# Kernel optimization log

Hardware: AMD Instinct MI355X
Metric: run time of the kernel (lower is better)

## Reference

```python
import math
import jax, jax.numpy as jnp
import numpy as np

N, L, D = 64, 128, 768          # batch, n_in capsules, feature dim
IN_DIM, OUT_DIM, N_OUT = 64, 64, 32
EPS = 1e-8

def _xavier(k, shape):
    # torch xavier_uniform: fan_in = shape[1]*prod(shape[2:]), fan_out = shape[0]*prod(shape[2:])
    rec = int(np.prod(shape[2:])) if len(shape) > 2 else 1
    fan_in, fan_out = shape[-2] * rec, shape[-1] * rec
    a = math.sqrt(6.0 / (fan_in + fan_out))
    return jax.random.uniform(k, shape, jnp.float32, -a, a)

def setup_inputs() -> dict:
    key = jax.random.key(0)
    ks = jax.random.split(key, 4)
    return {
        "x": jax.random.normal(ks[0], (N, L, D), jnp.float32),
        "Wscore": _xavier(ks[1], (L, D, 1)),
        "Bscore": jnp.zeros((L, 1, 1), jnp.float32),
        "Wcap": _xavier(ks[2], (L, D, IN_DIM)),
        "Bcap": jnp.zeros((L, 1, IN_DIM), jnp.float32),
        "Wvote": _xavier(ks[3], (L, N_OUT, IN_DIM, OUT_DIM)),
        "Bvote": jnp.zeros((L, N_OUT, 1, OUT_DIM), jnp.float32),
        "beta_use": jnp.zeros((L, 1, 1, 1), jnp.float32),
        "beta_ign": jnp.zeros((1, N_OUT, 1, 1), jnp.float32),
        "iters": 3,
    }

def reference(x, Wscore, Bscore, Wcap, Bcap, Wvote, Bvote, beta_use, beta_ign, iters):
    n_out = Wvote.shape[1]
    pi = jnp.asarray(math.pi, x.dtype)
    x_t = jnp.transpose(x, (1, 0, 2))                     # (L, N, D)
    a_in = jnp.matmul(x_t, Wscore) + Bscore               # (L, N, 1)
    mu_in = jax.nn.gelu(jnp.matmul(x_t, Wcap) + Bcap, approximate=False)  # (L, N, in_dim)
    f_a_in = jax.nn.sigmoid(a_in)[:, None, :, :]          # (L, 1, N, 1)
    # votes: (L, n_out, N, out_dim)
    V = jnp.einsum('lni,loij->lonj', mu_in, Wvote) + Bvote

    def em_step(R):
        D_use = f_a_in * R                                # (L, n_out, N, 1)
        D_ign = f_a_in - D_use
        a_out = jnp.sum(beta_use * D_use, axis=0) - jnp.sum(beta_ign * D_ign, axis=0)  # (n_out, N, 1)
        denom = jnp.sum(D_use, axis=0) + EPS              # (n_out, N, 1)
        mu_out = jnp.sum(D_use * V, axis=0) / denom       # (n_out, N, out_dim)
        var_out = jnp.sum(D_use * (V - mu_out[None]) ** 2, axis=0) / denom
        return a_out, mu_out, var_out

    R = jnp.full((1, n_out, 1, 1), 1.0 / n_out, dtype=x.dtype)
    a_out, mu_out, var_out = em_step(R)
    for _ in range(int(iters) - 1):
        # Gaussian log-likelihood of each vote under each output capsule
        log_p = (-jnp.sum((V - mu_out[None]) ** 2 / (2.0 * var_out[None] + EPS), axis=-1)
                 - 1.0 - 0.5 * pi
                 - 0.5 * jnp.sum(jnp.log(var_out[None] + EPS), axis=-1))   # (L, n_out, N)
        R = jax.nn.softmax(jax.nn.log_sigmoid(a_out)[None] + log_p[..., None], axis=1)
        a_out, mu_out, var_out = em_step(R)

    a_out = jnp.transpose(a_out[..., 0], (1, 0))          # (N, n_out)
    mu_out = jnp.transpose(mu_out, (1, 0, 2))             # (N, n_out, out_dim)
    return a_out, mu_out
```

## Files before the change

kernel.cpp:

```cpp
#include <hip/hip_runtime.h>
#include <math.h>

#define NB 64
#define LL 128
#define DD 768
#define ID 64
#define OD 64
#define NO 32
#define EPSF 1e-8f

typedef unsigned short ushort_t;
typedef __attribute__((ext_vector_type(8))) short bf16x8;
typedef __attribute__((ext_vector_type(4))) float f32x4;


__device__ __forceinline__ float gelu_exact(float v) {
  return 0.5f * v * (1.0f + erff(v * 0.70710678118654752440f));
}
__device__ __forceinline__ float sigmoidf_(float z) {
  return 1.0f / (1.0f + __expf(-z));
}
__device__ __forceinline__ unsigned short f2bf(float f) {
  unsigned u = __float_as_uint(f);
  unsigned r = (u + 0x7FFFu + ((u >> 16) & 1u)) >> 16;
  return (unsigned short)r;
}
__device__ __forceinline__ float bf2f(unsigned short s) {
  return __uint_as_float(((unsigned)s) << 16);
}

__global__ __launch_bounds__(256) void k0a_proj(
    const float* __restrict__ x, const float* __restrict__ Wscore,
    const float* __restrict__ Wcap,
    float* __restrict__ Cpart, float* __restrict__ apart)
{
  const int l  = blockIdx.x & 127;
  const int kc = blockIdx.x >> 7;
  const int t = threadIdx.x;
  const int tn = t >> 4;
  const int ti = t & 15;
  __shared__ float Xs[64][68];
  __shared__ float Ws[64][68];
  __shared__ float Ss[64];
  float C[4][4] = {{0.f}};
  float asum[4] = {0.f, 0.f, 0.f, 0.f};

  for (int kt = 0; kt < 2; ++kt) {
    const int kbase = kc * 128 + kt * 64;
#pragma unroll
    for (int r = 0; r < 4; ++r) {
      const int flat = r * 1024 + t * 4;
      const int p = flat >> 6, qq = flat & 63;
      *(float4*)&Xs[p][qq] = *(const float4*)&x[(p * LL + l) * DD + kbase + qq];
      *(float4*)&Ws[p][qq] = *(const float4*)&Wcap[(l * DD + kbase + p) * ID + qq];
    }
    if (t < 16)
      *(float4*)&Ss[4 * t] = *(const float4*)&Wscore[l * DD + kbase + 4 * t];
    __syncthreads();
#pragma unroll 8
    for (int k = 0; k < 64; ++k) {
      float av[4];
      av[0] = Xs[4 * tn + 0][k];
      av[1] = Xs[4 * tn + 1][k];
      av[2] = Xs[4 * tn + 2][k];
      av[3] = Xs[4 * tn + 3][k];
      const float4 b = *(const float4*)&Ws[k][4 * ti];
      const float sk = Ss[k];
#pragma unroll
      for (int a = 0; a < 4; ++a) {
        C[a][0] = fmaf(av[a], b.x, C[a][0]);
        C[a][1] = fmaf(av[a], b.y, C[a][1]);
        C[a][2] = fmaf(av[a], b.z, C[a][2]);
        C[a][3] = fmaf(av[a], b.w, C[a][3]);
        asum[a] = fmaf(av[a], sk, asum[a]);
      }
    }
    __syncthreads();
  }
#pragma unroll
  for (int a = 0; a < 4; ++a)
    *(float4*)&Cpart[kc * 524288 + (l * 64 + 4 * tn + a) * 64 + 4 * ti] =
        make_float4(C[a][0], C[a][1], C[a][2], C[a][3]);
  if (ti == 0) {
#pragma unroll
    for (int a = 0; a < 4; ++a)
      apart[kc * 8192 + l * 64 + 4 * tn + a] = asum[a];
  }
}

__global__ __launch_bounds__(256) void k0b_reduce(
    const float* __restrict__ Cpart, const float* __restrict__ Bcap,
    ushort_t* __restrict__ Ah, ushort_t* __restrict__ Al)
{
  const int e = (blockIdx.x * 256 + threadIdx.x) * 4;
  float4 s = *(const float4*)&Cpart[e];
#pragma unroll
  for (int kc = 1; kc < 6; ++kc) {
    const float4 p = *(const float4*)&Cpart[kc * 524288 + e];
    s.x += p.x; s.y += p.y; s.z += p.z; s.w += p.w;
  }
  const int l = e >> 12;
  const int col = e & 63;
  const float4 bc = *(const float4*)&Bcap[l * 64 + col];
  float m[4] = {gelu_exact(s.x + bc.x), gelu_exact(s.y + bc.y),
                gelu_exact(s.z + bc.z), gelu_exact(s.w + bc.w)};
  ushort4 h, lo;
  h.x = f2bf(m[0]); lo.x = f2bf(m[0] - bf2f(h.x));
  h.y = f2bf(m[1]); lo.y = f2bf(m[1] - bf2f(h.y));
  h.z = f2bf(m[2]); lo.z = f2bf(m[2] - bf2f(h.z));
  h.w = f2bf(m[3]); lo.w = f2bf(m[3] - bf2f(h.w));
  *(ushort4*)&Ah[e] = h;
  *(ushort4*)&Al[e] = lo;
}

__global__ __launch_bounds__(256) void k0c_fa(
    const float* __restrict__ apart, const float* __restrict__ Bscore,
    float* __restrict__ f_a)
{
  const int e = blockIdx.x * 256 + threadIdx.x;
  float s = 0.f;
#pragma unroll
  for (int kc = 0; kc < 6; ++kc) s += apart[kc * 8192 + e];
  const int l = e >> 6;
  f_a[e] = sigmoidf_(s + Bscore[l]);
}

__global__ __launch_bounds__(256) void k1_votes(
    const ushort_t* __restrict__ Ah, const ushort_t* __restrict__ Al,
    const float* __restrict__ Wvote, const float* __restrict__ Bvote,
    float* __restrict__ V)
{
  const int t = threadIdx.x;
  const int w = t >> 6;
  const int lane = t & 63;
  const int pair = blockIdx.x * 4 + w;
  const int l = pair >> 5;
  const int mr = lane & 15, q = lane >> 4;

  __shared__ unsigned HL_all[4][2048];
  unsigned* HL = HL_all[w];

  bf16x8 afh[2][4], afl[2][4];
#pragma unroll
  for (int ks = 0; ks < 2; ++ks)
#pragma unroll
    for (int mt = 0; mt < 4; ++mt) {
      const int off = l * 4096 + (16 * mt + mr) * 64 + ks * 32 + q * 8;
      afh[ks][mt] = *(const bf16x8*)&Ah[off];
      afl[ks][mt] = *(const bf16x8*)&Al[off];
    }

  const float* Wt = Wvote + (size_t)pair * 4096;

  f32x4 acc[4][4];
#pragma unroll
  for (int mt = 0; mt < 4; ++mt)
#pragma unroll
    for (int nt = 0; nt < 4; ++nt) {
      f32x4 z = {0.f, 0.f, 0.f, 0.f};
      acc[mt][nt] = z;
    }

  for (int ks = 0; ks < 2; ++ks) {
#pragma unroll
    for (int f = 0; f < 8; ++f) {
      const float4 v4 = *(const float4*)&Wt[ks * 2048 + f * 256 + lane * 4];
      const int ii = f * 4 + q;
      const int jc = (mr * 4) ^ ((ii & 8) << 1);
      const float e4[4] = {v4.x, v4.y, v4.z, v4.w};
      unsigned pk[4];
#pragma unroll
      for (int d = 0; d < 4; ++d) {
        const unsigned short hi = f2bf(e4[d]);
        const unsigned short lo = f2bf(e4[d] - bf2f(hi));
        pk[d] = (unsigned)hi | ((unsigned)lo << 16);
      }
      *(uint4*)&HL[ii * 64 + jc] = make_uint4(pk[0], pk[1], pk[2], pk[3]);
    }

#pragma unroll
    for (int nt = 0; nt < 4; ++nt) {
      const int j = 16 * nt + mr;
      unsigned wv[8];
#pragma unroll
      for (int d = 0; d < 8; ++d) {
        const int ii = q * 8 + d;
        wv[d] = HL[ii * 64 + (j ^ ((ii & 8) << 1))];
      }
      union { ushort_t u[8]; bf16x8 v; } bh, bl;
#pragma unroll
      for (int d = 0; d < 8; ++d) {
        bh.u[d] = (ushort_t)(wv[d] & 0xffffu);
        bl.u[d] = (ushort_t)(wv[d] >> 16);
      }
#pragma unroll
      for (int mt = 0; mt < 4; ++mt) {
        acc[mt][nt] = __builtin_amdgcn_mfma_f32_16x16x32_bf16(
            afh[ks][mt], bh.v, acc[mt][nt], 0, 0, 0);
        acc[mt][nt] = __builtin_amdgcn_mfma_f32_16x16x32_bf16(
            afh[ks][mt], bl.v, acc[mt][nt], 0, 0, 0);
        acc[mt][nt] = __builtin_amdgcn_mfma_f32_16x16x32_bf16(
            afl[ks][mt], bh.v, acc[mt][nt], 0, 0, 0);
      }
    }
  }

  float bv[4];
#pragma unroll
  for (int nt = 0; nt < 4; ++nt) bv[nt] = Bvote[pair * 64 + 16 * nt + mr];

#pragma unroll
  for (int mt = 0; mt < 4; ++mt)
#pragma unroll
    for (int r = 0; r < 4; ++r) {
      const int n = 16 * mt + 4 * q + r;
      const size_t base = (size_t)n * (LL * NO * OD) + (size_t)pair * 64;
#pragma unroll
      for (int nt = 0; nt < 4; ++nt)
        V[base + 16 * nt + mr] = acc[mt][nt][r] + bv[nt];
    }
}

__global__ __launch_bounds__(256) void k3_em(
    const float* __restrict__ V, const float* __restrict__ f_a,
    const float* __restrict__ beta_use, const float* __restrict__ mu_s,
    const float* __restrict__ i2v_s, const float* __restrict__ cterm,
    float* __restrict__ S1p, float* __restrict__ S2p,
    float* __restrict__ dnp, float* __restrict__ aUp, const int mode)
{
  const int n = blockIdx.x >> 3;
  const int c = blockIdx.x & 7;
  const int t = threadIdx.x;
  const int o = t >> 3, q = t & 7;
  __shared__ float ttl[8][32];

  float mu8[8], iv8[8];
  float ct = 0.f;
  if (mode) {
    const float4 a0 = *(const float4*)&mu_s[n * 2048 + t * 8];
    const float4 a1 = *(const float4*)&mu_s[n * 2048 + t * 8 + 4];
    mu8[0] = a0.x; mu8[1] = a0.y; mu8[2] = a0.z; mu8[3] = a0.w;
    mu8[4] = a1.x; mu8[5] = a1.y; mu8[6] = a1.z; mu8[7] = a1.w;
    const float4 b0 = *(const float4*)&i2v_s[n * 2048 + t * 8];
    const float4 b1 = *(const float4*)&i2v_s[n * 2048 + t * 8 + 4];
    iv8[0] = b0.x; iv8[1] = b0.y; iv8[2] = b0.z; iv8[3] = b0.w;
    iv8[4] = b1.x; iv8[5] = b1.y; iv8[6] = b1.z; iv8[7] = b1.w;
    ct = cterm[n * NO + o];
  }
  float aS1[8] = {0.f, 0.f, 0.f, 0.f, 0.f, 0.f, 0.f, 0.f};
  float aS2[8] = {0.f, 0.f, 0.f, 0.f, 0.f, 0.f, 0.f, 0.f};
  float dn = 0.f, aU = 0.f;

  for (int g = 0; g < 4; ++g) {
    const int lb = c * 16 + g * 4;
    float Vv[4][8], fa4[4], bu4[4], tt4[4];
#pragma unroll
    for (int u = 0; u < 4; ++u) {
      const int l = lb + u;
      const float4 v0 = *(const float4*)&V[((size_t)n * LL + l) * 2048 + t * 8];
      const float4 v1 = *(const float4*)&V[((size_t)n * LL + l) * 2048 + t * 8 + 4];
      Vv[u][0] = v0.x; Vv[u][1] = v0.y; Vv[u][2] = v0.z; Vv[u][3] = v0.w;
      Vv[u][4] = v1.x; Vv[u][5] = v1.y; Vv[u][6] = v1.z; Vv[u][7] = v1.w;
      fa4[u] = f_a[l * NB + n];
      bu4[u] = beta_use[l];
    }
    if (mode) {
#pragma unroll
      for (int u = 0; u < 4; ++u) {
        float s2 = 0.f;
#pragma unroll
        for (int k = 0; k < 8; ++k) {
          const float d = Vv[u][k] - mu8[k];
          s2 = fmaf(d * d, iv8[k], s2);
        }
        s2 += __shfl_xor(s2, 1);
        s2 += __shfl_xor(s2, 2);
        s2 += __shfl_xor(s2, 4);
        tt4[u] = ct - s2;
      }
      const int sb = (g & 1) * 4;
      if (q == 0) {
#pragma unroll
        for (int u = 0; u < 4; ++u) ttl[sb + u][o] = tt4[u];
      }
      __syncthreads();
#pragma unroll
      for (int u = 0; u < 4; ++u) {
        const float vv = ttl[sb + u][t & 31];
        float m = vv;
#pragma unroll
        for (int msk = 1; msk <= 16; msk <<= 1) m = fmaxf(m, __shfl_xor(m, msk));
        float z = __expf(vv - m);
#pragma unroll
        for (int msk = 1; msk <= 16; msk <<= 1) z += __shfl_xor(z, msk);
        const float wgt = fa4[u] * __expf(tt4[u] - m) / z;
        dn += wgt;
        aU = fmaf(bu4[u], wgt, aU);
#pragma unroll
        for (int k = 0; k < 8; ++k) {
          const float d = Vv[u][k] - mu8[k];
          aS1[k] = fmaf(wgt, Vv[u][k], aS1[k]);
          aS2[k] = fmaf(wgt, d * d, aS2[k]);
        }
      }
    } else {
#pragma unroll
      for (int u = 0; u < 4; ++u) {
        const float wgt = fa4[u] * (1.0f / NO);
        dn += wgt;
        aU = fmaf(bu4[u], wgt, aU);
#pragma unroll
        for (int k = 0; k < 8; ++k) {
          aS1[k] = fmaf(wgt, Vv[u][k], aS1[k]);
          aS2[k] = fmaf(wgt * Vv[u][k], Vv[u][k], aS2[k]);
        }
      }
    }
  }
  const int base = ((c * NB + n) * NO + o) * OD + q * 8;
  *(float4*)&S1p[base]     = make_float4(aS1[0], aS1[1], aS1[2], aS1[3]);
  *(float4*)&S1p[base + 4] = make_float4(aS1[4], aS1[5], aS1[6], aS1[7]);
  *(float4*)&S2p[base]     = make_float4(aS2[0], aS2[1], aS2[2], aS2[3]);
  *(float4*)&S2p[base + 4] = make_float4(aS2[4], aS2[5], aS2[6], aS2[7]);
  if (q == 0) {
    dnp[(c * NB + n) * NO + o] = dn;
    aUp[(c * NB + n) * NO + o] = aU;
  }
}

__global__ __launch_bounds__(256) void k4_fin23(
    const float* __restrict__ S1p, const float* __restrict__ S2p,
    const float* __restrict__ dnp, const float* __restrict__ aUp,
    const float* __restrict__ f_a, const float* __restrict__ beta_ign,
    float* __restrict__ mu_s, float* __restrict__ i2v_s, float* __restrict__ cterm,
    float* __restrict__ out, const int final_iter, const int first)
{
  const int n = blockIdx.x;
  const int t = threadIdx.x;
  const int o = t >> 3, q = t & 7;
  const int j0 = q * 8;
  __shared__ float rA[128];
  if (t < 128) rA[t] = f_a[t * NB + n];
  __syncthreads();
  for (int s = 64; s >= 1; s >>= 1) {
    if (t < s) rA[t] += rA[t + s];
    __syncthreads();
  }
  const float Fsum = rA[0];

  float dn = 0.f, aU = 0.f;
#pragma unroll
  for (int cc = 0; cc < 8; ++cc) {
    dn += dnp[(cc * NB + n) * NO + o];
    aU += aUp[(cc * NB + n) * NO + o];
  }
  const float S0 = dn;
  const float denom = dn + EPSF;
  const float inv_den = 1.0f / denom;

  float S1[8], S2[8];
#pragma unroll
  for (int k = 0; k < 8; ++k) { S1[k] = 0.f; S2[k] = 0.f; }
  for (int cc = 0; cc < 8; ++cc) {
    const int base = ((cc * NB + n) * NO + o) * OD + j0;
    const float4 u0 = *(const float4*)&S1p[base];
    const float4 u1 = *(const float4*)&S1p[base + 4];
    const float4 w0 = *(const float4*)&S2p[base];
    const float4 w1 = *(const float4*)&S2p[base + 4];
    S1[0] += u0.x; S1[1] += u0.y; S1[2] += u0.z; S1[3] += u0.w;
    S1[4] += u1.x; S1[5] += u1.y; S1[6] += u1.z; S1[7] += u1.w;
    S2[0] += w0.x; S2[1] += w0.y; S2[2] += w0.z; S2[3] += w0.w;
    S2[4] += w1.x; S2[5] += w1.y; S2[6] += w1.z; S2[7] += w1.w;
  }
  float mup[8];
  if (first) {
#pragma unroll
    for (int k = 0; k < 8; ++k) mup[k] = 0.f;
  } else {
    const float4 a0 = *(const float4*)&mu_s[n * 2048 + t * 8];
    const float4 a1 = *(const float4*)&mu_s[n * 2048 + t * 8 + 4];
    mup[0] = a0.x; mup[1] = a0.y; mup[2] = a0.z; mup[3] = a0.w;
    mup[4] = a1.x; mup[5] = a1.y; mup[6] = a1.z; mup[7] = a1.w;
  }
  const float aout = aU - beta_ign[o] * (Fsum - dn);

  float mu[8], i2v[8];
  float lacc = 0.f;
#pragma unroll
  for (int k = 0; k < 8; ++k) {
    mu[k] = S1[k] * inv_den;
    const float dd = mu[k] - mup[k];
    float varn = S2[k] - 2.0f * dd * (S1[k] - mup[k] * S0) + dd * dd * S0;
    float var = fmaxf(varn * inv_den, 0.0f);
    i2v[k] = 1.0f / (2.0f * var + EPSF);
    lacc += logf(var + EPSF);
  }
  if (final_iter) {
    if (q == 0) out[n * NO + o] = aout;
    *(float4*)&out[2048 + n * 2048 + t * 8]     = make_float4(mu[0], mu[1], mu[2], mu[3]);
    *(float4*)&out[2048 + n * 2048 + t * 8 + 4] = make_float4(mu[4], mu[5], mu[6], mu[7]);
  } else {
    *(float4*)&mu_s[n * 2048 + t * 8]      = make_float4(mu[0], mu[1], mu[2], mu[3]);
    *(float4*)&mu_s[n * 2048 + t * 8 + 4]  = make_float4(mu[4], mu[5], mu[6], mu[7]);
    *(float4*)&i2v_s[n * 2048 + t * 8]     = make_float4(i2v[0], i2v[1], i2v[2], i2v[3]);
    *(float4*)&i2v_s[n * 2048 + t * 8 + 4] = make_float4(i2v[4], i2v[5], i2v[6], i2v[7]);
    lacc += __shfl_xor(lacc, 1);
    lacc += __shfl_xor(lacc, 2);
    lacc += __shfl_xor(lacc, 4);
    const float lsg = fminf(aout, 0.0f) - log1pf(__expf(-fabsf(aout)));
    if (q == 0) cterm[n * NO + o] = lsg - 0.5f * lacc;
  }
}

extern "C" void kernel_launch(void* const* d_in, const int* in_sizes, int n_in,
                              void* d_out, int out_size, void* d_ws, size_t ws_size,
                              hipStream_t stream) {
  const float* x        = (const float*)d_in[0];
  const float* Wscore   = (const float*)d_in[1];
  const float* Bscore   = (const float*)d_in[2];
  const float* Wcap     = (const float*)d_in[3];
  const float* Bcap     = (const float*)d_in[4];
  const float* Wvote    = (const float*)d_in[5];
  const float* Bvote    = (const float*)d_in[6];
  const float* beta_use = (const float*)d_in[7];
  const float* beta_ign = (const float*)d_in[8];
  float* out = (float*)d_out;

  float* ws     = (float*)d_ws;
  float* V      = ws;
  float* Cpart  = ws;
  float* apart  = ws + 3145728;
  ushort_t* Ah  = (ushort_t*)(ws + 16777216);
  ushort_t* Al  = Ah + 524288;
  float* f_a    = ws + 16777216 + 524288;
  float* S1p    = f_a + 8192;
  float* S2p    = S1p + 1048576;
  float* dnp    = S2p + 1048576;
  float* aUp    = dnp + 16384;
  float* mu_s   = aUp + 16384;
  float* i2v_s  = mu_s + 131072;
  float* ct     = i2v_s + 131072;
  const size_t need = (size_t)(16777216 + 524288 + 8192 + 2 * 1048576 +
                               2 * 16384 + 2 * 131072 + 2048) * sizeof(float);
  if (ws_size < need) return;

  k0a_proj<<<768, 256, 0, stream>>>(x, Wscore, Wcap, Cpart, apart);
  k0b_reduce<<<512, 256, 0, stream>>>(Cpart, Bcap, Ah, Al);
  k0c_fa<<<32, 256, 0, stream>>>(apart, Bscore, f_a);
  k1_votes<<<1024, 256, 0, stream>>>(Ah, Al, Wvote, Bvote, V);
  k3_em<<<512, 256, 0, stream>>>(V, f_a, beta_use, mu_s, i2v_s, ct, S1p, S2p, dnp, aUp, 0);
  k4_fin23<<<64, 256, 0, stream>>>(S1p, S2p, dnp, aUp, f_a, beta_ign, mu_s, i2v_s, ct, out, 0, 1);
  k3_em<<<512, 256, 0, stream>>>(V, f_a, beta_use, mu_s, i2v_s, ct, S1p, S2p, dnp, aUp, 1);
  k4_fin23<<<64, 256, 0, stream>>>(S1p, S2p, dnp, aUp, f_a, beta_ign, mu_s, i2v_s, ct, out, 0, 0);
  k3_em<<<512, 256, 0, stream>>>(V, f_a, beta_use, mu_s, i2v_s, ct, S1p, S2p, dnp, aUp, 1);
  k4_fin23<<<64, 256, 0, stream>>>(S1p, S2p, dnp, aUp, f_a, beta_ign, mu_s, i2v_s, ct, out, 1, 0);
}
```

Before: 249.6 us.

## Pre-swizzle capsule activations for MFMA loads and stage vote stores through LDS

New measurement: 244.9 us. Within noise of the previous version (-1.9%).

```diff
diff --git a/kernel.cpp b/kernel.cpp
--- a/kernel.cpp
+++ b/kernel.cpp
@@ -100,8 +100,9 @@
     s.x += p.x; s.y += p.y; s.z += p.z; s.w += p.w;
   }
   const int l = e >> 12;
-  const int col = e & 63;
-  const float4 bc = *(const float4*)&Bcap[l * 64 + col];
+  const int n = (e >> 6) & 63;
+  const int i0 = e & 63;
+  const float4 bc = *(const float4*)&Bcap[l * 64 + i0];
   float m[4] = {gelu_exact(s.x + bc.x), gelu_exact(s.y + bc.y),
                 gelu_exact(s.z + bc.z), gelu_exact(s.w + bc.w)};
   ushort4 h, lo;
@@ -109,8 +110,10 @@
   h.y = f2bf(m[1]); lo.y = f2bf(m[1] - bf2f(h.y));
   h.z = f2bf(m[2]); lo.z = f2bf(m[2] - bf2f(h.z));
   h.w = f2bf(m[3]); lo.w = f2bf(m[3] - bf2f(h.w));
-  *(ushort4*)&Ah[e] = h;
-  *(ushort4*)&Al[e] = lo;
+  const int off = l * 4096 + (i0 >> 5) * 2048 + (n >> 4) * 512 + (n & 15) * 32 +
+                  ((i0 >> 3) & 3) * 8 + (i0 & 7);
+  *(ushort4*)&Ah[off] = h;
+  *(ushort4*)&Al[off] = lo;
 }
 
 __global__ __launch_bounds__(256) void k0c_fa(
@@ -141,11 +144,12 @@
   unsigned* HL = HL_all[w];
 
   bf16x8 afh[2][4], afl[2][4];
+  const int afoff = (lane & 15) * 32 + (lane >> 4) * 8;
 #pragma unroll
   for (int ks = 0; ks < 2; ++ks)
 #pragma unroll
     for (int mt = 0; mt < 4; ++mt) {
-      const int off = l * 4096 + (16 * mt + mr) * 64 + ks * 32 + q * 8;
+      const int off = l * 4096 + ks * 2048 + mt * 512 + afoff;
       afh[ks][mt] = *(const bf16x8*)&Ah[off];
       afl[ks][mt] = *(const bf16x8*)&Al[off];
     }
@@ -209,16 +213,25 @@
 #pragma unroll
   for (int nt = 0; nt < 4; ++nt) bv[nt] = Bvote[pair * 64 + 16 * nt + mr];
 
-#pragma unroll
-  for (int mt = 0; mt < 4; ++mt)
-#pragma unroll
-    for (int r = 0; r < 4; ++r) {
-      const int n = 16 * mt + 4 * q + r;
-      const size_t base = (size_t)n * (LL * NO * OD) + (size_t)pair * 64;
-#pragma unroll
-      for (int nt = 0; nt < 4; ++nt)
-        V[base + 16 * nt + mr] = acc[mt][nt][r] + bv[nt];
-    }
+  float* T = (float*)HL;
+  const int c4 = (lane & 15) * 4;
+  const int qh = lane >> 4;
+#pragma unroll
+  for (int mt = 0; mt < 4; ++mt) {
+#pragma unroll
+    for (int nt = 0; nt < 4; ++nt)
+#pragma unroll
+      for (int r = 0; r < 4; ++r)
+        T[(4 * q + r) * 68 + 16 * nt + mr] = acc[mt][nt][r] + bv[nt];
+#pragma unroll
+    for (int rr = 0; rr < 4; ++rr) {
+      const int rw = 4 * rr + qh;
+      const float4 vv = *(const float4*)&T[rw * 68 + c4];
+      const size_t base =
+          (size_t)(16 * mt + rw) * (LL * NO * OD) + (size_t)pair * 64 + c4;
+      *(float4*)&V[base] = vv;
+    }
+  }
 }
 
 __global__ __launch_bounds__(256) void k3_em(
```
